# Optimization experiments

Measured on AMD Instinct MI355X. Metric: run time of the kernel, lower is better.

The kernel has to match this reference:

```python
import jax, jax.numpy as jnp
import numpy as np
from jax import lax

B, T, V, E, H = 512, 256, 128, 64, 64  # H = per-direction hidden (hidden_dim//2)


def setup_inputs() -> dict:
    key = jax.random.key(0)
    ks = jax.random.split(key, 25)
    x_raw = jax.random.randint(ks[0], (B, T), 1, V)
    lengths = jax.random.randint(ks[1], (B,), T // 2, T + 1)
    x = jnp.where(jnp.arange(T)[None, :] < lengths[:, None], x_raw, 0)  # pad_idx=0
    tags = jax.random.randint(ks[2], (B, T), 0, V)
    s = 0.1
    n = lambda k, sh: s * jax.random.normal(k, sh, dtype=jnp.float32)
    inp = {"x": x, "tags": tags, "emb": n(ks[3], (V, E))}
    names = ["w_ih_l0", "w_hh_l0", "b_ih_l0", "b_hh_l0", "w_ih_l0r", "w_hh_l0r", "b_ih_l0r", "b_hh_l0r",
             "w_ih_l1", "w_hh_l1", "b_ih_l1", "b_hh_l1", "w_ih_l1r", "w_hh_l1r", "b_ih_l1r", "b_hh_l1r"]
    shapes = [(4 * H, E), (4 * H, H), (4 * H,), (4 * H,), (4 * H, E), (4 * H, H), (4 * H,), (4 * H,),
              (4 * H, 2 * H), (4 * H, H), (4 * H,), (4 * H,), (4 * H, 2 * H), (4 * H, H), (4 * H,), (4 * H,)]
    for i, (nm, sh) in enumerate(zip(names, shapes)):
        inp[nm] = n(ks[4 + i], sh)
    inp["lin_w"] = n(ks[20], (V, 2 * H))
    inp["lin_b"] = n(ks[21], (V,))
    inp["crf_start"] = n(ks[22], (V,))
    inp["crf_end"] = n(ks[23], (V,))
    inp["crf_trans"] = n(ks[24], (V, V))
    return inp


def _lstm_dir(x, wih, whh, bih, bhh, reverse):
    # x: [B,T,D]; PyTorch gate order i,f,g,o
    xs = jnp.swapaxes(x, 0, 1)  # [T,B,D]
    if reverse:
        xs = xs[::-1]
    Bn, Hn = x.shape[0], whh.shape[1]
    pre = jnp.einsum('tbd,gd->tbg', xs, wih) + bih + bhh  # input projection once

    def step(carry, p):
        h, c = carry
        g = p + h @ whh.T
        i, f, gg, o = jnp.split(g, 4, axis=-1)
        c = jax.nn.sigmoid(f) * c + jax.nn.sigmoid(i) * jnp.tanh(gg)
        h = jax.nn.sigmoid(o) * jnp.tanh(c)
        return (h, c), h

    init = (jnp.zeros((Bn, Hn), x.dtype), jnp.zeros((Bn, Hn), x.dtype))
    _, hs = lax.scan(step, init, pre)
    if reverse:
        hs = hs[::-1]
    return jnp.swapaxes(hs, 0, 1)  # [B,T,H]


def _bilstm_layer(x, wf, hf, bif, bhf, wb, hb, bib, bhb):
    return jnp.concatenate([_lstm_dir(x, wf, hf, bif, bhf, False),
                            _lstm_dir(x, wb, hb, bib, bhb, True)], axis=-1)


def _crf_nll(emissions, tags, mask, start, end, trans):
    # torchcrf forward with reduction='mean'; returns -llh.mean()
    maskf = mask.astype(emissions.dtype)
    em_t = jnp.take_along_axis(emissions, tags[..., None], axis=2)[..., 0]  # [B,T]
    score = start[tags[:, 0]] + em_t[:, 0]
    trans_sc = trans[tags[:, :-1], tags[:, 1:]]  # [B,T-1]
    score = score + jnp.sum((trans_sc + em_t[:, 1:]) * maskf[:, 1:], axis=1)
    last_idx = jnp.sum(mask.astype(jnp.int32), axis=1) - 1
    last_tags = jnp.take_along_axis(tags, last_idx[:, None], axis=1)[:, 0]
    score = score + end[last_tags]
    # log-partition via scan over time
    alpha0 = start[None, :] + emissions[:, 0]  # [B,V]

    def step(alpha, inp):
        em_i, m_i = inp  # [B,V], [B]
        nxt = jax.nn.logsumexp(alpha[:, :, None] + trans[None, :, :] + em_i[:, None, :], axis=1)
        return jnp.where(m_i[:, None], nxt, alpha), None

    alpha, _ = lax.scan(step, alpha0,
                        (jnp.swapaxes(emissions[:, 1:], 0, 1), jnp.swapaxes(mask[:, 1:], 0, 1)))
    partition = jax.nn.logsumexp(alpha + end[None, :], axis=1)
    return -jnp.mean(score - partition)


def reference(x, tags, emb,
              w_ih_l0, w_hh_l0, b_ih_l0, b_hh_l0, w_ih_l0r, w_hh_l0r, b_ih_l0r, b_hh_l0r,
              w_ih_l1, w_hh_l1, b_ih_l1, b_hh_l1, w_ih_l1r, w_hh_l1r, b_ih_l1r, b_hh_l1r,
              lin_w, lin_b, crf_start, crf_end, crf_trans):
    mask = x != 0
    h = emb[x]  # [B,T,E]
    h = _bilstm_layer(h, w_ih_l0, w_hh_l0, b_ih_l0, b_hh_l0, w_ih_l0r, w_hh_l0r, b_ih_l0r, b_hh_l0r)
    h = _bilstm_layer(h, w_ih_l1, w_hh_l1, b_ih_l1, b_hh_l1, w_ih_l1r, w_hh_l1r, b_ih_l1r, b_hh_l1r)
    # dropout in eval mode (identity)
    emissions = jnp.einsum('btd,vd->btv', h, lin_w) + lin_b  # [B,T,V]
    return _crf_nll(emissions, tags, mask, crf_start, crf_end, crf_trans)
```

## Files before the change

### kernel.cpp

```cpp
#include <hip/hip_runtime.h>

#define BB 512
#define TT 256
#define VV 128
#define EE 64
#define HH 64
#define GG 256
#define DD 128
#define NN1 512

typedef unsigned short ushort8_t __attribute__((ext_vector_type(8)));
typedef _Float16 h8v __attribute__((ext_vector_type(8)));
typedef _Float16 h4v __attribute__((ext_vector_type(4)));
typedef float f4v __attribute__((ext_vector_type(4)));

__device__ __forceinline__ float rcpf(float x){ return __builtin_amdgcn_rcpf(x); }
__device__ __forceinline__ float sigf(float x){ return rcpf(1.0f + __expf(-x)); }
__device__ __forceinline__ float tanhfast(float x){ return 1.0f - 2.0f*rcpf(__expf(2.0f*x)+1.0f); }
__device__ __forceinline__ unsigned short f2h(float f){
  union { _Float16 h; unsigned short u; } cv; cv.h = (_Float16)f; return cv.u;
}

#define STEP_BARRIER() { \
  __builtin_amdgcn_sched_barrier(0); \
  asm volatile("s_waitcnt lgkmcnt(0)"); \
  __builtin_amdgcn_s_barrier(); \
  __builtin_amdgcn_sched_barrier(0); \
}

__device__ __forceinline__ int gqp(int n){
  return (n & 256) | ((n & 63) << 2) | ((n >> 6) & 3);
}

template<int L> struct PVT { typedef h4v T; };
template<>      struct PVT<0> { typedef f4v T; };

__global__ void k_prep(const float* __restrict__ emb,
    const float* __restrict__ wih0f, const float* __restrict__ bih0f, const float* __restrict__ bhh0f,
    const float* __restrict__ wih0b, const float* __restrict__ bih0b, const float* __restrict__ bhh0b,
    const float* __restrict__ wih1f, const float* __restrict__ bih1f, const float* __restrict__ bhh1f,
    const float* __restrict__ wih1b, const float* __restrict__ bih1b, const float* __restrict__ bhh1b,
    const float* __restrict__ whh0f, const float* __restrict__ whh0b,
    const float* __restrict__ whh1f, const float* __restrict__ whh1b,
    const float* __restrict__ lin_w, const float* __restrict__ trans, const float* __restrict__ endv,
    float* __restrict__ P0f, float* __restrict__ P0b,
    unsigned short* __restrict__ wB1, unsigned short* __restrict__ linB,
    float* __restrict__ bias1, unsigned short* __restrict__ etH, float* __restrict__ eend,
    unsigned short* __restrict__ whhH)
{
  int bid = blockIdx.x, tid = threadIdx.x;
  if (bid < 256){
    int d = bid >> 7, v = bid & 127;
    const float* wih = d ? wih0b : wih0f;
    const float* bi  = d ? bih0b : bih0f;
    const float* bh  = d ? bhh0b : bhh0f;
    float* P0 = d ? P0b : P0f;
    __shared__ __align__(16) float er[64];
    if (tid < 64) er[tid] = emb[v*64 + tid];
    __syncthreads();
    float acc = bi[tid] + bh[tid];
    const float4* w4 = (const float4*)(wih + tid*64);
    const float4* e4 = (const float4*)er;
    #pragma unroll
    for (int k=0;k<16;k++){
      float4 w = w4[k]; float4 e = e4[k];
      acc += w.x*e.x + w.y*e.y + w.z*e.z + w.w*e.w;
    }
    P0[v*GG + ((tid & 63)<<2) + (tid >> 6)] = acc;
  } else if (bid < 320){
    int e = ((bid-256)*256 + tid)*4;
    int n = e >> 7, k = e & 127;
    const float* w = (n < 256) ? (wih1f + n*128 + k) : (wih1b + (n-256)*128 + k);
    ushort4 o; o.x=f2h(w[0]); o.y=f2h(w[1]); o.z=f2h(w[2]); o.w=f2h(w[3]);
    *(ushort4*)(wB1 + gqp(n)*128 + k) = o;
  } else if (bid < 336){
    int e = ((bid-320)*256 + tid)*4;
    const float* w = lin_w + e;
    ushort4 o; o.x=f2h(w[0]); o.y=f2h(w[1]); o.z=f2h(w[2]); o.w=f2h(w[3]);
    *(ushort4*)(linB + e) = o;
  } else if (bid < 400){
    int idx = (bid-336)*256 + tid;
    int i = idx >> 7, jj = idx & 127;
    etH[jj*128 + i] = f2h(__expf(trans[idx]));
  } else if (bid == 400){
    for (int i = tid; i < 512; i += 256){
      int d = i >> 8, gg = i & 255;
      bias1[gqp(i)] = d ? (bih1b[gg]+bhh1b[gg]) : (bih1f[gg]+bhh1f[gg]);
    }
    if (tid < 128) eend[tid] = expf(endv[tid]);
  } else {
    int blk = bid - 401;
    int arr = blk >> 2;
    int off = (blk & 3)*4096 + tid*16;
    const float* srcs[4] = { whh0f, whh0b, whh1f, whh1b };
    const float* s = srcs[arr];
    #pragma unroll
    for (int u=0;u<16;u+=4){
      float4 v = *(const float4*)(s + off + u);
      unsigned short* dst = whhH + arr*16384 + off + u;
      dst[0]=f2h(v.x); dst[1]=f2h(v.y); dst[2]=f2h(v.z); dst[3]=f2h(v.w);
    }
  }
}

#define LSTM_STEP(T_, P_, OFF_) { \
  const int rb_ = (T_)&1, wb_ = rb_^1; \
  h8v a0_ = *(const h8v*)(hb + rb_*2048 + rdA0); \
  h8v a1_ = *(const h8v*)(hb + rb_*2048 + rdA1); \
  f4v acc_[4]; \
  _Pragma("unroll") \
  for (int gt=0; gt<4; gt++){ \
    f4v zz; zz[0]=0.f; zz[1]=0.f; zz[2]=0.f; zz[3]=0.f; \
    zz = __builtin_amdgcn_mfma_f32_16x16x32_f16(a0_, bf[gt][0], zz, 0,0,0); \
    acc_[gt] = __builtin_amdgcn_mfma_f32_16x16x32_f16(a1_, bf[gt][1], zz, 0,0,0); \
  } \
  _Pragma("unroll") \
  for (int rr=0;rr<2;rr++){ \
    const int r = rr*2; \
    const float gi = acc_[0][r] + (float)P_[rr][0]; \
    const float gf = acc_[1][r] + (float)P_[rr][1]; \
    const float gc = acc_[2][r] + (float)P_[rr][2]; \
    const float go = acc_[3][r] + (float)P_[rr][3]; \
    const float cn = sigf(gf)*c[rr] + sigf(gi)*tanhfast(gc); \
    const float hn = sigf(go)*tanhfast(cn); \
    c[rr] = cn; \
    const _Float16 hh = (_Float16)hn; \
    *(_Float16*)(hb + wb_*2048 + wAddr[rr]) = hh; \
    *(_Float16*)((char*)hout + hOff[rr]) = hh; \
    hOff[rr] += hstep; \
  } \
  if ((T_)+2 < TT){ \
    if constexpr (LAYER == 0){ \
      const int tp_ = dir ? (TT-3-(T_)) : ((T_)+2); \
      _Pragma("unroll") \
      for (int rr=0;rr<2;rr++){ \
        const int xv_ = xs[(2*q+rr)*256 + tp_]; \
        P_[rr] = *(const f4v*)(P0 + xv_*GG + (j<<2)); \
      } \
    } else { \
      _Pragma("unroll") \
      for (int rr=0;rr<2;rr++){ \
        OFF_[rr] += pstep2; \
        P_[rr] = *(const h4v*)((const char*)pre1 + OFF_[rr]); \
      } \
    } \
  } \
  STEP_BARRIER(); \
}

template<int LAYER>
__global__ __launch_bounds__(256)
void k_lstm(const int* __restrict__ x, const float* __restrict__ P0f,
            const float* __restrict__ P0b, const _Float16* __restrict__ pre1,
            const _Float16* __restrict__ whhL, _Float16* __restrict__ hout)
{
  const int bid = blockIdx.x;
  const int dir = bid >> 6;
  const int b0  = (bid & 63) * 8;
  const int tid = threadIdx.x;
  const int wv  = tid >> 6;
  const int lane = tid & 63;
  const int l16 = lane & 15, q = lane >> 4;
  const int j = wv*16 + l16;

  const _Float16* whh = whhL + dir*(GG*HH);
  h8v bf[4][2];
  #pragma unroll
  for (int gt=0; gt<4; gt++){
    const int n = gt*64 + j;
    #pragma unroll
    for (int ks=0; ks<2; ks++)
      bf[gt][ks] = *(const h8v*)(whh + n*HH + ks*32 + q*8);
  }

  __shared__ __align__(16) _Float16 hsm[2][16*64];
  __shared__ int xs[(LAYER==0) ? 8*256 : 2];
  char* hb = (char*)&hsm[0][0];
  *(float4*)(hb + tid*16) = make_float4(0.f,0.f,0.f,0.f);
  *(float4*)(hb + 4096 + tid*16) = make_float4(0.f,0.f,0.f,0.f);
  if (LAYER == 0){
    #pragma unroll
    for (int i=0;i<2;i++)
      ((int4*)xs)[tid + i*256] = ((const int4*)(x + b0*TT))[tid + i*256];
  }
  __syncthreads();

  const float* P0 = dir ? P0b : P0f;
  const int tt0 = dir ? TT-1 : 0;
  const int tt1 = dir ? TT-2 : 1;
  const int hstep  = dir ? -(DD*2) : (DD*2);
  const int pstep2 = dir ? -(NN1*4) : (NN1*4);

  const int swz = (l16 & 7) << 4;
  const int rdA0 = (l16*128 +  0 + q*16) ^ swz;
  const int rdA1 = (l16*128 + 64 + q*16) ^ swz;
  int wAddr[2];
  unsigned hOff[2];
  #pragma unroll
  for (int rr=0;rr<2;rr++){
    const int m = 4*q + rr*2;
    wAddr[rr] = (m*128 + j*2) ^ ((m&7)<<4);
    hOff[rr]  = (unsigned)((((b0+2*q+rr)*TT + tt0)*DD + dir*HH + j)*2);
  }

  typename PVT<LAYER>::T pA[2], pB[2];
  unsigned offA[2], offB[2];
  if constexpr (LAYER == 0){
    #pragma unroll
    for (int rr=0;rr<2;rr++){
      const int x0 = xs[(2*q+rr)*256 + tt0];
      const int x1 = xs[(2*q+rr)*256 + tt1];
      pA[rr] = *(const f4v*)(P0 + x0*GG + (j<<2));
      pB[rr] = *(const f4v*)(P0 + x1*GG + (j<<2));
    }
  } else {
    #pragma unroll
    for (int rr=0;rr<2;rr++){
      offA[rr] = (unsigned)(((((b0+2*q+rr)*TT + tt0)*NN1) + dir*256 + (j<<2))*2);
      offB[rr] = (unsigned)(((((b0+2*q+rr)*TT + tt1)*NN1) + dir*256 + (j<<2))*2);
      pA[rr] = *(const h4v*)((const char*)pre1 + offA[rr]);
      pB[rr] = *(const h4v*)((const char*)pre1 + offB[rr]);
    }
  }
  float c[2] = {0.f,0.f};

  for (int t=0; t<TT; t+=2){
    LSTM_STEP(t,   pA, offA);
    LSTM_STEP(t+1, pB, offB);
  }
}

__global__ __launch_bounds__(256, 2)
void k_gemm_mfma(const unsigned short* __restrict__ A, const unsigned short* __restrict__ Bw,
                 const float* __restrict__ bias, void* __restrict__ C,
                 _Float16* __restrict__ EP,
                 const int N, const int of16)
{
  __shared__ __align__(16) unsigned short As[128*136];
  __shared__ __align__(16) unsigned short Bs[64*136];
  const int tid = threadIdx.x;
  const size_t m0 = (size_t)blockIdx.y * 128;
  const int n0 = blockIdx.x * 64;
  #pragma unroll
  for (int i=0;i<8;i++){
    int idx = tid + i*256;
    int r = idx >> 4, c = idx & 15;
    *(ushort8_t*)(As + r*136 + c*8) = *(const ushort8_t*)(A + (m0+r)*128 + c*8);
  }
  #pragma unroll
  for (int i=0;i<4;i++){
    int idx = tid + i*256;
    int r = idx >> 4, c = idx & 15;
    *(ushort8_t*)(Bs + r*136 + c*8) = *(const ushort8_t*)(Bw + (size_t)(n0+r)*128 + c*8);
  }
  __syncthreads();
  const int lane = tid & 63, wid = tid >> 6;
  const int wm = (wid & 1) * 64, wn = (wid >> 1) * 32;
  const int l16 = lane & 15, q = lane >> 4;
  f4v acc[4][2];
  #pragma unroll
  for (int i=0;i<4;i++){
    #pragma unroll
    for (int jj=0;jj<2;jj++){ acc[i][jj][0]=0.f; acc[i][jj][1]=0.f; acc[i][jj][2]=0.f; acc[i][jj][3]=0.f; }
  }
  #pragma unroll
  for (int ks=0; ks<4; ks++){
    const int kb = ks*32 + q*8;
    h8v a[4], b[2];
    #pragma unroll
    for (int mt=0;mt<4;mt++) a[mt] = *(const h8v*)(As + (wm + mt*16 + l16)*136 + kb);
    #pragma unroll
    for (int nt=0;nt<2;nt++) b[nt] = *(const h8v*)(Bs + (wn + nt*16 + l16)*136 + kb);
    #pragma unroll
    for (int mt=0;mt<4;mt++){
      #pragma unroll
      for (int nt=0;nt<2;nt++){
        acc[mt][nt] = __builtin_amdgcn_mfma_f32_16x16x32_f16(a[mt], b[nt], acc[mt][nt], 0, 0, 0);
      }
    }
  }
  #pragma unroll
  for (int mt=0;mt<4;mt++){
    #pragma unroll
    for (int nt=0;nt<2;nt++){
      int col = n0 + wn + nt*16 + l16;
      float bv = bias[col];
      #pragma unroll
      for (int r=0;r<4;r++){
        size_t row = m0 + wm + mt*16 + q*4 + r;
        float v = acc[mt][nt][r] + bv;
        if (of16){
          ((_Float16*)C)[row*N + col] = (_Float16)v;
        } else {
          ((float*)C)[row*N + col] = v;
          EP[row*128 + col] = (_Float16)__expf(v);
        }
      }
    }
  }
}

__global__ void k_score(const int* __restrict__ x, const int* __restrict__ tags,
                        const float* __restrict__ em, const float* __restrict__ startv,
                        const float* __restrict__ endv, const float* __restrict__ trans,
                        float* __restrict__ score)
{
  int b = blockIdx.x, lane = threadIdx.x;
  float s = 0.f; int cnt = 0;
  for (int t = lane; t < TT; t += 64){
    int xv = x[b*TT + t];
    int m = (xv != 0);
    cnt += m;
    if (t >= 1 && m){
      int tp = tags[b*TT + t - 1], tc = tags[b*TT + t];
      s += trans[tp*VV + tc] + em[(size_t)(b*TT + t)*VV + tc];
    }
  }
  #pragma unroll
  for (int o=32;o>0;o>>=1){ s += __shfl_down(s,o,64); cnt += __shfl_down(cnt,o,64); }
  if (lane==0){
    int t0 = tags[b*TT];
    s += startv[t0] + em[(size_t)(b*TT)*VV + t0];
    int lt = tags[b*TT + cnt - 1];
    s += endv[lt];
    score[b] = s;
  }
}

#define CRF_STEP(T_, EM_, EOFF_) { \
  const int rb_ = ((T_)+1)&1, wb_ = (T_)&1; \
  h8v af_[4]; \
  _Pragma("unroll") \
  for (int ks=0;ks<4;ks++) af_[ks] = *(const h8v*)(alp + rb_*2176 + l16*136 + ks*32 + q*8); \
  f4v zac_; zac_[0]=0.f; zac_[1]=0.f; zac_[2]=0.f; zac_[3]=0.f; \
  _Pragma("unroll") \
  for (int ks=0;ks<4;ks++) zac_ = __builtin_amdgcn_mfma_f32_16x16x32_f16(bones, af_[ks], zac_, 0,0,0); \
  f4v acc_[4]; \
  _Pragma("unroll") \
  for (int nt=0;nt<4;nt++){ \
    f4v zz; zz[0]=0.f; zz[1]=0.f; zz[2]=0.f; zz[3]=0.f; \
    _Pragma("unroll") \
    for (int ks=0;ks<4;ks++) zz = __builtin_amdgcn_mfma_f32_16x16x32_f16(bf[nt][ks], af_[ks], zz, 0,0,0); \
    acc_[nt] = zz; \
  } \
  const float iz_ = rcpf(zac_[0]); \
  const bool act_ = (T_) < lenB; \
  if (act_) Lacc += __logf(zac_[0]); \
  _Pragma("unroll") \
  for (int nt=0;nt<4;nt++){ \
    h4v hw_; \
    _Pragma("unroll") \
    for (int r=0;r<4;r++) hw_[r] = (_Float16)(acc_[nt][r] * (float)EM_[nt][r] * iz_); \
    if (act_) *(h4v*)(alp + wb_*2176 + l16*136 + c0 + nt*16 + q*4) = hw_; \
  } \
  if ((T_)+2 < TT){ \
    _Pragma("unroll") \
    for (int nt=0;nt<4;nt++){ \
      EOFF_[nt] += 512; \
      EM_[nt] = *(const h4v*)((const char*)eem + EOFF_[nt]); \
    } \
  } \
  STEP_BARRIER(); \
}

__global__ __launch_bounds__(128)
void k_crf(const int* __restrict__ x, const float* __restrict__ em,
           const _Float16* __restrict__ eem, const _Float16* __restrict__ etH,
           const float* __restrict__ startv, const float* __restrict__ eend,
           float* __restrict__ part)
{
  const int b0 = blockIdx.x * 16;
  const int tid = threadIdx.x;
  const int wv = tid >> 6;
  const int lane = tid & 63;
  const int l16 = lane & 15, q = lane >> 4;
  const int c0 = wv * 64;

  h8v bf[4][4];
  #pragma unroll
  for (int nt=0; nt<4; nt++){
    #pragma unroll
    for (int ks=0; ks<4; ks++)
      bf[nt][ks] = *(const h8v*)(etH + (size_t)(c0 + nt*16 + l16)*128 + ks*32 + q*8);
  }
  h8v bones;
  #pragma unroll
  for (int i=0;i<8;i++) bones[i] = (_Float16)1.0f;

  __shared__ __align__(16) _Float16 alpha[2][16*136];
  __shared__ __align__(16) float fred[32];
  __shared__ int lenS[16];
  _Float16* alp = &alpha[0][0];

  {
    const int row = tid >> 3, seg = tid & 7;
    const int* xr = x + (b0+row)*TT + seg*32;
    int cnt = 0;
    #pragma unroll
    for (int u=0;u<32;u+=4){
      int4 v4 = *(const int4*)(xr + u);
      cnt += (v4.x!=0) + (v4.y!=0) + (v4.z!=0) + (v4.w!=0);
    }
    cnt += __shfl_xor(cnt, 1, 64);
    cnt += __shfl_xor(cnt, 2, 64);
    cnt += __shfl_xor(cnt, 4, 64);
    if (seg == 0) lenS[row] = cnt;
  }
  __syncthreads();
  int ML = 0;
  #pragma unroll
  for (int i=0;i<16;i++){ int li = lenS[i]; ML = li > ML ? li : ML; }
  const int lenB = lenS[l16];

  float Lacc = 0.f;
  #pragma unroll
  for (int nt=0;nt<4;nt++){
    const int j0 = c0 + nt*16 + q*4;
    f4v em0 = *(const f4v*)(em + ((size_t)(b0+l16)*TT)*VV + j0);
    f4v st  = *(const f4v*)(startv + j0);
    h4v a0;
    #pragma unroll
    for (int r=0;r<4;r++) a0[r] = (_Float16)__expf(st[r] + em0[r]);
    *(h4v*)(alp + l16*136 + j0) = a0;
  }
  h4v EMA[4], EMB[4];
  unsigned eOffA[4], eOffB[4];
  #pragma unroll
  for (int nt=0;nt<4;nt++){
    eOffA[nt] = (unsigned)(((((b0+l16)*TT + 1)*128) + c0 + nt*16 + q*4)*2);
    eOffB[nt] = eOffA[nt] + 256u;
    EMA[nt] = *(const h4v*)((const char*)eem + eOffA[nt]);
    EMB[nt] = *(const h4v*)((const char*)eem + eOffB[nt]);
  }
  STEP_BARRIER();

  int t = 1;
  for (; t+1 < ML; t += 2){
    CRF_STEP(t,   EMA, eOffA);
    CRF_STEP(t+1, EMB, eOffB);
  }
  if (t < ML){ CRF_STEP(t, EMA, eOffA); }

  {
    const int lb = (lenB-1) & 1;
    float ps = 0.f;
    #pragma unroll
    for (int nt=0;nt<4;nt++){
      const int j0 = c0 + nt*16 + q*4;
      h4v av = *(const h4v*)(alp + lb*2176 + l16*136 + j0);
      f4v ev = *(const f4v*)(eend + j0);
      #pragma unroll
      for (int r=0;r<4;r++) ps += (float)av[r] * ev[r];
    }
    ps += __shfl_xor(ps, 16, 64);
    ps += __shfl_xor(ps, 32, 64);
    if (q == 0) fred[l16*2 + wv] = ps;
    __syncthreads();
    if (wv == 0 && q == 0){
      float2 p2 = *(const float2*)(&fred[l16*2]);
      part[b0 + l16] = Lacc + __logf(p2.x + p2.y);
    }
  }
}

__global__ void k_final(const float* __restrict__ part, const float* __restrict__ score,
                        float* __restrict__ out)
{
  __shared__ float red[8];
  int tid = threadIdx.x;
  float v = part[tid] - score[tid];
  #pragma unroll
  for (int o=32;o>0;o>>=1) v += __shfl_down(v,o,64);
  if ((tid&63)==0) red[tid>>6] = v;
  __syncthreads();
  if (tid==0){
    float s = 0.f;
    #pragma unroll
    for (int i=0;i<8;i++) s += red[i];
    out[0] = s / (float)BB;
  }
}

extern "C" void kernel_launch(void* const* d_in, const int* in_sizes, int n_in,
                              void* d_out, int out_size, void* d_ws, size_t ws_size,
                              hipStream_t stream)
{
  const int*   x        = (const int*)d_in[0];
  const int*   tags     = (const int*)d_in[1];
  const float* emb      = (const float*)d_in[2];
  const float* w_ih_l0  = (const float*)d_in[3];
  const float* w_hh_l0  = (const float*)d_in[4];
  const float* b_ih_l0  = (const float*)d_in[5];
  const float* b_hh_l0  = (const float*)d_in[6];
  const float* w_ih_l0r = (const float*)d_in[7];
  const float* w_hh_l0r = (const float*)d_in[8];
  const float* b_ih_l0r = (const float*)d_in[9];
  const float* b_hh_l0r = (const float*)d_in[10];
  const float* w_ih_l1  = (const float*)d_in[11];
  const float* w_hh_l1  = (const float*)d_in[12];
  const float* b_ih_l1  = (const float*)d_in[13];
  const float* b_hh_l1  = (const float*)d_in[14];
  const float* w_ih_l1r = (const float*)d_in[15];
  const float* w_hh_l1r = (const float*)d_in[16];
  const float* b_ih_l1r = (const float*)d_in[17];
  const float* b_hh_l1r = (const float*)d_in[18];
  const float* lin_w    = (const float*)d_in[19];
  const float* lin_b    = (const float*)d_in[20];
  const float* crf_start= (const float*)d_in[21];
  const float* crf_end  = (const float*)d_in[22];
  const float* crf_trans= (const float*)d_in[23];

  char* ws = (char*)d_ws;
  float*          P0f    = (float*)(ws + 0);
  float*          P0b    = (float*)(ws + 131072);
  unsigned short* wB1    = (unsigned short*)(ws + 262144);
  unsigned short* linB   = (unsigned short*)(ws + 393216);
  float*          bias1  = (float*)(ws + 425984);
  unsigned short* etH    = (unsigned short*)(ws + 428032);
  float*          eend   = (float*)(ws + 460800);
  float*          scoreA = (float*)(ws + 461312);
  float*          partA  = (float*)(ws + 463360);
  unsigned short* whhH   = (unsigned short*)(ws + 465408);
  const size_t MB1 = 1ull<<20;
  _Float16* hbuf = (_Float16*)(ws + MB1);
  _Float16* pre1 = (_Float16*)(ws + MB1 + 33554432ull);
  float*    em   = (float*)(ws + MB1 + 33554432ull);
  _Float16* eemP = (_Float16*)(ws + MB1 + 33554432ull + 67108864ull);

  k_prep<<<dim3(417), dim3(256), 0, stream>>>(
      emb, w_ih_l0,b_ih_l0,b_hh_l0, w_ih_l0r,b_ih_l0r,b_hh_l0r,
      w_ih_l1,b_ih_l1,b_hh_l1, w_ih_l1r,b_ih_l1r,b_hh_l1r,
      w_hh_l0, w_hh_l0r, w_hh_l1, w_hh_l1r,
      lin_w, crf_trans, crf_end,
      P0f,P0b,wB1,linB,bias1,etH,eend,whhH);

  k_lstm<0><<<dim3(128), dim3(256), 0, stream>>>(
      x, P0f, P0b, pre1, (const _Float16*)whhH, hbuf);

  k_gemm_mfma<<<dim3(8,1024), dim3(256), 0, stream>>>(
      (const unsigned short*)hbuf, wB1, bias1, (void*)pre1, (_Float16*)nullptr, 512, 1);

  k_lstm<1><<<dim3(128), dim3(256), 0, stream>>>(
      x, P0f, P0b, pre1, (const _Float16*)whhH + 2*GG*HH, hbuf);

  k_gemm_mfma<<<dim3(2,1024), dim3(256), 0, stream>>>(
      (const unsigned short*)hbuf, linB, lin_b, (void*)em, eemP, 128, 0);

  k_score<<<dim3(512), dim3(64), 0, stream>>>(
      x, tags, em, crf_start, crf_end, crf_trans, scoreA);

  k_crf<<<dim3(32), dim3(128), 0, stream>>>(
      x, em, eemP, (const _Float16*)etH, crf_start, eend, partA);

  k_final<<<dim3(1), dim3(512), 0, stream>>>(partA, scoreA, (float*)d_out);
}
```

Measured before the change: 530.8 us.

## Give each CRF wave all tag columns so it needs no block barriers

The CRF forward recursion is restructured so that one wavefront owns 16 batch rows across all 128 tags, instead of two waves splitting the tag columns and syncing through a block barrier every step. The alpha buffer becomes a single per-wave LDS slice updated in place, and sequence lengths and the max length are reduced with wave shuffles rather than shared memory. The final reduction across waves and its __syncthreads are also removed. In exchange, each wave issues twice as many MFMAs per step on a serial dependency chain, and packing 8 waves into each of only 4 blocks concentrates the work on fewer CUs, so waves compete for the same SIMDs.

Measured after the change: 845.8 us. 59.3% more time.

```diff
diff --git a/kernel.cpp b/kernel.cpp
--- a/kernel.cpp
+++ b/kernel.cpp
@@ -328,16 +328,15 @@
 }
 
 #define CRF_STEP(T_, EM_, EOFF_) { \
-  const int rb_ = ((T_)+1)&1, wb_ = (T_)&1; \
   h8v af_[4]; \
   _Pragma("unroll") \
-  for (int ks=0;ks<4;ks++) af_[ks] = *(const h8v*)(alp + rb_*2176 + l16*136 + ks*32 + q*8); \
+  for (int ks=0;ks<4;ks++) af_[ks] = *(const h8v*)(alp + l16*136 + ks*32 + q*8); \
   f4v zac_; zac_[0]=0.f; zac_[1]=0.f; zac_[2]=0.f; zac_[3]=0.f; \
   _Pragma("unroll") \
   for (int ks=0;ks<4;ks++) zac_ = __builtin_amdgcn_mfma_f32_16x16x32_f16(bones, af_[ks], zac_, 0,0,0); \
-  f4v acc_[4]; \
+  f4v acc_[8]; \
   _Pragma("unroll") \
-  for (int nt=0;nt<4;nt++){ \
+  for (int nt=0;nt<8;nt++){ \
     f4v zz; zz[0]=0.f; zz[1]=0.f; zz[2]=0.f; zz[3]=0.f; \
     _Pragma("unroll") \
     for (int ks=0;ks<4;ks++) zz = __builtin_amdgcn_mfma_f32_16x16x32_f16(bf[nt][ks], af_[ks], zz, 0,0,0); \
@@ -347,75 +346,71 @@
   const bool act_ = (T_) < lenB; \
   if (act_) Lacc += __logf(zac_[0]); \
   _Pragma("unroll") \
-  for (int nt=0;nt<4;nt++){ \
+  for (int nt=0;nt<8;nt++){ \
     h4v hw_; \
     _Pragma("unroll") \
     for (int r=0;r<4;r++) hw_[r] = (_Float16)(acc_[nt][r] * (float)EM_[nt][r] * iz_); \
-    if (act_) *(h4v*)(alp + wb_*2176 + l16*136 + c0 + nt*16 + q*4) = hw_; \
+    if (act_) *(h4v*)(alp + l16*136 + nt*16 + q*4) = hw_; \
   } \
   if ((T_)+2 < TT){ \
+    EOFF_ += 512u; \
     _Pragma("unroll") \
-    for (int nt=0;nt<4;nt++){ \
-      EOFF_[nt] += 512; \
-      EM_[nt] = *(const h4v*)((const char*)eem + EOFF_[nt]); \
-    } \
+    for (int nt=0;nt<8;nt++) EM_[nt] = *(const h4v*)((const char*)eem + EOFF_ + nt*32); \
   } \
-  STEP_BARRIER(); \
-}
-
-__global__ __launch_bounds__(128)
+  __builtin_amdgcn_sched_barrier(0); \
+}
+
+__global__ __launch_bounds__(512, 2)
 void k_crf(const int* __restrict__ x, const float* __restrict__ em,
            const _Float16* __restrict__ eem, const _Float16* __restrict__ etH,
            const float* __restrict__ startv, const float* __restrict__ eend,
            float* __restrict__ part)
 {
-  const int b0 = blockIdx.x * 16;
   const int tid = threadIdx.x;
-  const int wv = tid >> 6;
+  const int w   = tid >> 6;
   const int lane = tid & 63;
+  const int b0 = (blockIdx.x*8 + w) * 16;
   const int l16 = lane & 15, q = lane >> 4;
-  const int c0 = wv * 64;
-
-  h8v bf[4][4];
-  #pragma unroll
-  for (int nt=0; nt<4; nt++){
+
+  h8v bf[8][4];
+  #pragma unroll
+  for (int nt=0; nt<8; nt++){
     #pragma unroll
     for (int ks=0; ks<4; ks++)
-      bf[nt][ks] = *(const h8v*)(etH + (size_t)(c0 + nt*16 + l16)*128 + ks*32 + q*8);
+      bf[nt][ks] = *(const h8v*)(etH + (size_t)(nt*16 + l16)*128 + ks*32 + q*8);
   }
   h8v bones;
   #pragma unroll
   for (int i=0;i<8;i++) bones[i] = (_Float16)1.0f;
 
-  __shared__ __align__(16) _Float16 alpha[2][16*136];
-  __shared__ __align__(16) float fred[32];
-  __shared__ int lenS[16];
-  _Float16* alp = &alpha[0][0];
-
+  __shared__ __align__(16) _Float16 alpha[8][16*136];
+  _Float16* alp = &alpha[w][0];
+
+  int lenB, MLw;
   {
-    const int row = tid >> 3, seg = tid & 7;
-    const int* xr = x + (b0+row)*TT + seg*32;
+    const int row = lane >> 2, seg = lane & 3;
+    const int* xr = x + (b0+row)*TT + seg*64;
     int cnt = 0;
     #pragma unroll
-    for (int u=0;u<32;u+=4){
+    for (int u=0;u<64;u+=4){
       int4 v4 = *(const int4*)(xr + u);
       cnt += (v4.x!=0) + (v4.y!=0) + (v4.z!=0) + (v4.w!=0);
     }
     cnt += __shfl_xor(cnt, 1, 64);
     cnt += __shfl_xor(cnt, 2, 64);
-    cnt += __shfl_xor(cnt, 4, 64);
-    if (seg == 0) lenS[row] = cnt;
-  }
-  __syncthreads();
-  int ML = 0;
-  #pragma unroll
-  for (int i=0;i<16;i++){ int li = lenS[i]; ML = li > ML ? li : ML; }
-  const int lenB = lenS[l16];
+    lenB = __shfl(cnt, l16*4, 64);
+    int m = cnt, m2;
+    m2 = __shfl_xor(m, 4, 64);  m = m2 > m ? m2 : m;
+    m2 = __shfl_xor(m, 8, 64);  m = m2 > m ? m2 : m;
+    m2 = __shfl_xor(m, 16, 64); m = m2 > m ? m2 : m;
+    m2 = __shfl_xor(m, 32, 64); m = m2 > m ? m2 : m;
+    MLw = m;
+  }
 
   float Lacc = 0.f;
   #pragma unroll
-  for (int nt=0;nt<4;nt++){
-    const int j0 = c0 + nt*16 + q*4;
+  for (int nt=0;nt<8;nt++){
+    const int j0 = nt*16 + q*4;
     f4v em0 = *(const f4v*)(em + ((size_t)(b0+l16)*TT)*VV + j0);
     f4v st  = *(const f4v*)(startv + j0);
     h4v a0;
@@ -423,43 +418,35 @@
     for (int r=0;r<4;r++) a0[r] = (_Float16)__expf(st[r] + em0[r]);
     *(h4v*)(alp + l16*136 + j0) = a0;
   }
-  h4v EMA[4], EMB[4];
-  unsigned eOffA[4], eOffB[4];
-  #pragma unroll
-  for (int nt=0;nt<4;nt++){
-    eOffA[nt] = (unsigned)(((((b0+l16)*TT + 1)*128) + c0 + nt*16 + q*4)*2);
-    eOffB[nt] = eOffA[nt] + 256u;
-    EMA[nt] = *(const h4v*)((const char*)eem + eOffA[nt]);
-    EMB[nt] = *(const h4v*)((const char*)eem + eOffB[nt]);
-  }
-  STEP_BARRIER();
+  h4v EMA[8], EMB[8];
+  unsigned eOffA = (unsigned)((((b0+l16)*TT + 1)*128 + q*4)*2);
+  unsigned eOffB = eOffA + 256u;
+  #pragma unroll
+  for (int nt=0;nt<8;nt++){
+    EMA[nt] = *(const h4v*)((const char*)eem + eOffA + nt*32);
+    EMB[nt] = *(const h4v*)((const char*)eem + eOffB + nt*32);
+  }
 
   int t = 1;
-  for (; t+1 < ML; t += 2){
+  for (; t+1 < MLw; t += 2){
     CRF_STEP(t,   EMA, eOffA);
     CRF_STEP(t+1, EMB, eOffB);
   }
-  if (t < ML){ CRF_STEP(t, EMA, eOffA); }
+  if (t < MLw){ CRF_STEP(t, EMA, eOffA); }
 
   {
-    const int lb = (lenB-1) & 1;
     float ps = 0.f;
     #pragma unroll
-    for (int nt=0;nt<4;nt++){
-      const int j0 = c0 + nt*16 + q*4;
-      h4v av = *(const h4v*)(alp + lb*2176 + l16*136 + j0);
+    for (int nt=0;nt<8;nt++){
+      const int j0 = nt*16 + q*4;
+      h4v av = *(const h4v*)(alp + l16*136 + j0);
       f4v ev = *(const f4v*)(eend + j0);
       #pragma unroll
       for (int r=0;r<4;r++) ps += (float)av[r] * ev[r];
     }
     ps += __shfl_xor(ps, 16, 64);
     ps += __shfl_xor(ps, 32, 64);
-    if (q == 0) fred[l16*2 + wv] = ps;
-    __syncthreads();
-    if (wv == 0 && q == 0){
-      float2 p2 = *(const float2*)(&fred[l16*2]);
-      part[b0 + l16] = Lacc + __logf(p2.x + p2.y);
-    }
+    if (q == 0) part[b0 + l16] = Lacc + __logf(ps);
   }
 }
 
@@ -549,7 +536,7 @@
   k_score<<<dim3(512), dim3(64), 0, stream>>>(
       x, tags, em, crf_start, crf_end, crf_trans, scoreA);
 
-  k_crf<<<dim3(32), dim3(128), 0, stream>>>(
+  k_crf<<<dim3(4), dim3(512), 0, stream>>>(
       x, em, eemP, (const _Float16*)etH, crf_start, eend, partA);
 
   k_final<<<dim3(1), dim3(512), 0, stream>>>(partA, scoreA, (float*)d_out);
```

## Halve batch rows per LSTM block to double block count across CUs

Applied to the files above, without the earlier changes.

The LSTM recurrence kernels now give each block 4 batch rows instead of 8 and launch 256 blocks instead of 128. Each thread handles one batch row instead of two, so the gate math, hidden-state stores and pre-activation prefetch per serial step are halved. This spreads the serial recurrence over more of the device's CUs to shorten the per-step critical path, at the cost of MFMA tiles that are only partly used (16-row tiles with 4 valid rows) and more redundant weight loads.

Result: faster. 482.5 us (median of 2 runs) (-9.1%).

```diff
diff --git a/kernel.cpp b/kernel.cpp
--- a/kernel.cpp
+++ b/kernel.cpp
@@ -114,35 +114,27 @@
     zz = __builtin_amdgcn_mfma_f32_16x16x32_f16(a0_, bf[gt][0], zz, 0,0,0); \
     acc_[gt] = __builtin_amdgcn_mfma_f32_16x16x32_f16(a1_, bf[gt][1], zz, 0,0,0); \
   } \
-  _Pragma("unroll") \
-  for (int rr=0;rr<2;rr++){ \
-    const int r = rr*2; \
-    const float gi = acc_[0][r] + (float)P_[rr][0]; \
-    const float gf = acc_[1][r] + (float)P_[rr][1]; \
-    const float gc = acc_[2][r] + (float)P_[rr][2]; \
-    const float go = acc_[3][r] + (float)P_[rr][3]; \
-    const float cn = sigf(gf)*c[rr] + sigf(gi)*tanhfast(gc); \
+  { \
+    const float gi = acc_[0][0] + (float)P_[0]; \
+    const float gf = acc_[1][0] + (float)P_[1]; \
+    const float gc = acc_[2][0] + (float)P_[2]; \
+    const float go = acc_[3][0] + (float)P_[3]; \
+    const float cn = sigf(gf)*c0s + sigf(gi)*tanhfast(gc); \
     const float hn = sigf(go)*tanhfast(cn); \
-    c[rr] = cn; \
+    c0s = cn; \
     const _Float16 hh = (_Float16)hn; \
-    *(_Float16*)(hb + wb_*2048 + wAddr[rr]) = hh; \
-    *(_Float16*)((char*)hout + hOff[rr]) = hh; \
-    hOff[rr] += hstep; \
+    *(_Float16*)(hb + wb_*2048 + wAddr) = hh; \
+    *(_Float16*)((char*)hout + hOff) = hh; \
+    hOff += hstep; \
   } \
   if ((T_)+2 < TT){ \
     if constexpr (LAYER == 0){ \
       const int tp_ = dir ? (TT-3-(T_)) : ((T_)+2); \
-      _Pragma("unroll") \
-      for (int rr=0;rr<2;rr++){ \
-        const int xv_ = xs[(2*q+rr)*256 + tp_]; \
-        P_[rr] = *(const f4v*)(P0 + xv_*GG + (j<<2)); \
-      } \
+      const int xv_ = xs[q*256 + tp_]; \
+      P_ = *(const f4v*)(P0 + xv_*GG + (j<<2)); \
     } else { \
-      _Pragma("unroll") \
-      for (int rr=0;rr<2;rr++){ \
-        OFF_[rr] += pstep2; \
-        P_[rr] = *(const h4v*)((const char*)pre1 + OFF_[rr]); \
-      } \
+      OFF_ += pstep2; \
+      P_ = *(const h4v*)((const char*)pre1 + OFF_); \
     } \
   } \
   STEP_BARRIER(); \
@@ -155,8 +147,8 @@
             const _Float16* __restrict__ whhL, _Float16* __restrict__ hout)
 {
   const int bid = blockIdx.x;
-  const int dir = bid >> 6;
-  const int b0  = (bid & 63) * 8;
+  const int dir = bid >> 7;
+  const int b0  = (bid & 127) * 4;
   const int tid = threadIdx.x;
   const int wv  = tid >> 6;
   const int lane = tid & 63;
@@ -174,14 +166,12 @@
   }
 
   __shared__ __align__(16) _Float16 hsm[2][16*64];
-  __shared__ int xs[(LAYER==0) ? 8*256 : 2];
+  __shared__ int xs[(LAYER==0) ? 4*256 : 2];
   char* hb = (char*)&hsm[0][0];
   *(float4*)(hb + tid*16) = make_float4(0.f,0.f,0.f,0.f);
   *(float4*)(hb + 4096 + tid*16) = make_float4(0.f,0.f,0.f,0.f);
   if (LAYER == 0){
-    #pragma unroll
-    for (int i=0;i<2;i++)
-      ((int4*)xs)[tid + i*256] = ((const int4*)(x + b0*TT))[tid + i*256];
+    ((int4*)xs)[tid] = ((const int4*)(x + b0*TT))[tid];
   }
   __syncthreads();
 
@@ -194,35 +184,24 @@
   const int swz = (l16 & 7) << 4;
   const int rdA0 = (l16*128 +  0 + q*16) ^ swz;
   const int rdA1 = (l16*128 + 64 + q*16) ^ swz;
-  int wAddr[2];
-  unsigned hOff[2];
-  #pragma unroll
-  for (int rr=0;rr<2;rr++){
-    const int m = 4*q + rr*2;
-    wAddr[rr] = (m*128 + j*2) ^ ((m&7)<<4);
-    hOff[rr]  = (unsigned)((((b0+2*q+rr)*TT + tt0)*DD + dir*HH + j)*2);
-  }
-
-  typename PVT<LAYER>::T pA[2], pB[2];
-  unsigned offA[2], offB[2];
+  const int m = 4*q;
+  const int wAddr = (m*128 + j*2) ^ ((m&7)<<4);
+  unsigned hOff = (unsigned)((((b0+q)*TT + tt0)*DD + dir*HH + j)*2);
+
+  typename PVT<LAYER>::T pA, pB;
+  unsigned offA = 0, offB = 0;
   if constexpr (LAYER == 0){
-    #pragma unroll
-    for (int rr=0;rr<2;rr++){
-      const int x0 = xs[(2*q+rr)*256 + tt0];
-      const int x1 = xs[(2*q+rr)*256 + tt1];
-      pA[rr] = *(const f4v*)(P0 + x0*GG + (j<<2));
-      pB[rr] = *(const f4v*)(P0 + x1*GG + (j<<2));
-    }
+    const int x0 = xs[q*256 + tt0];
+    const int x1 = xs[q*256 + tt1];
+    pA = *(const f4v*)(P0 + x0*GG + (j<<2));
+    pB = *(const f4v*)(P0 + x1*GG + (j<<2));
   } else {
-    #pragma unroll
-    for (int rr=0;rr<2;rr++){
-      offA[rr] = (unsigned)(((((b0+2*q+rr)*TT + tt0)*NN1) + dir*256 + (j<<2))*2);
-      offB[rr] = (unsigned)(((((b0+2*q+rr)*TT + tt1)*NN1) + dir*256 + (j<<2))*2);
-      pA[rr] = *(const h4v*)((const char*)pre1 + offA[rr]);
-      pB[rr] = *(const h4v*)((const char*)pre1 + offB[rr]);
-    }
-  }
-  float c[2] = {0.f,0.f};
+    offA = (unsigned)(((((b0+q)*TT + tt0)*NN1) + dir*256 + (j<<2))*2);
+    offB = (unsigned)(((((b0+q)*TT + tt1)*NN1) + dir*256 + (j<<2))*2);
+    pA = *(const h4v*)((const char*)pre1 + offA);
+    pB = *(const h4v*)((const char*)pre1 + offB);
+  }
+  float c0s = 0.f;
 
   for (int t=0; t<TT; t+=2){
     LSTM_STEP(t,   pA, offA);
@@ -534,13 +513,13 @@
       lin_w, crf_trans, crf_end,
       P0f,P0b,wB1,linB,bias1,etH,eend,whhH);
 
-  k_lstm<0><<<dim3(128), dim3(256), 0, stream>>>(
+  k_lstm<0><<<dim3(256), dim3(256), 0, stream>>>(
       x, P0f, P0b, pre1, (const _Float16*)whhH, hbuf);
 
   k_gemm_mfma<<<dim3(8,1024), dim3(256), 0, stream>>>(
       (const unsigned short*)hbuf, wB1, bias1, (void*)pre1, (_Float16*)nullptr, 512, 1);
 
-  k_lstm<1><<<dim3(128), dim3(256), 0, stream>>>(
+  k_lstm<1><<<dim3(256), dim3(256), 0, stream>>>(
       x, P0f, P0b, pre1, (const _Float16*)whhH + 2*GG*HH, hbuf);
 
   k_gemm_mfma<<<dim3(2,1024), dim3(256), 0, stream>>>(
```
